# Optimization experiments

Measured on AMD Instinct MI355X. Metric: run time of the kernel, lower is better.

## Reference

```python
import jax, jax.numpy as jnp
import numpy as np

CLIP_MEAN = np.array([0.48145466, 0.4578275, 0.40821073], dtype=np.float32)
CLIP_STD = np.array([0.26862954, 0.26130258, 0.27577711], dtype=np.float32)


def setup_inputs() -> dict:
    key = jax.random.key(0)
    k_img, k_x, k_y, k_w, k_h = jax.random.split(key, 5)
    C, H, W = 3, 2048, 2048
    N = 256
    MAXB, MINB = 320, 32  # bbox side range in pixels
    img = jax.random.uniform(k_img, (C, H, W), dtype=jnp.float32, minval=0.0, maxval=255.0)
    x0 = jax.random.randint(k_x, (N,), 0, W - MAXB)
    y0 = jax.random.randint(k_y, (N,), 0, H - MAXB)
    bw = jax.random.randint(k_w, (N,), MINB, MAXB)
    bh = jax.random.randint(k_h, (N,), MINB, MAXB)
    bboxes = jnp.stack([x0, y0, x0 + bw, y0 + bh], axis=1).astype(jnp.int32)  # [N,4] xyxy
    return {
        "img": img,
        "mean": jnp.asarray(CLIP_MEAN),
        "std": jnp.asarray(CLIP_STD),
        "bboxes": bboxes,
        "size": 224,
    }


def _crop_resize(img, bboxes, size):
    """Batched crop-to-bbox + short-edge resize + center-crop == sample the
    central square (side = min(bh, bw)) of each bbox onto a size x size grid
    with bilinear interpolation. img: [C,H,W] float, bboxes: [N,4] int xyxy.
    Returns [N,C,size,size]."""
    C, H, W = img.shape
    b = bboxes.astype(jnp.float32)
    x0, y0, x1, y1 = b[:, 0], b[:, 1], b[:, 2], b[:, 3]
    side = jnp.minimum(x1 - x0, y1 - y0)            # [N]
    cx, cy = (x0 + x1) * 0.5, (y0 + y1) * 0.5        # [N]
    # output pixel j -> source coord start + (j+0.5)*scale - 0.5 (torch resize convention)
    grid = (jnp.arange(size, dtype=jnp.float32) + 0.5) / size  # [S]
    sx = (cx - side * 0.5)[:, None] + grid[None, :] * side[:, None] - 0.5  # [N,S]
    sy = (cy - side * 0.5)[:, None] + grid[None, :] * side[:, None] - 0.5  # [N,S]
    sx = jnp.clip(sx, 0.0, W - 1.0)
    sy = jnp.clip(sy, 0.0, H - 1.0)
    ix0 = jnp.floor(sx).astype(jnp.int32)
    iy0 = jnp.floor(sy).astype(jnp.int32)
    ix1 = jnp.minimum(ix0 + 1, W - 1)
    iy1 = jnp.minimum(iy0 + 1, H - 1)
    wx = (sx - ix0.astype(jnp.float32))[None, :, None, :]  # broadcast over C and y
    wy = (sy - iy0.astype(jnp.float32))[None, :, :, None]  # broadcast over C and x
    # gathers -> [C,N,S,S]
    p00 = img[:, iy0[:, :, None], ix0[:, None, :]]
    p01 = img[:, iy0[:, :, None], ix1[:, None, :]]
    p10 = img[:, iy1[:, :, None], ix0[:, None, :]]
    p11 = img[:, iy1[:, :, None], ix1[:, None, :]]
    top = p00 + wx * (p01 - p00)
    bot = p10 + wx * (p11 - p10)
    patches = top + wy * (bot - top)                 # [C,N,S,S]
    return jnp.transpose(patches, (1, 0, 2, 3))      # [N,C,S,S]


def reference(img, mean, std, bboxes, size):
    patches = _crop_resize(img, bboxes, size)        # [N,3,S,S]
    patches = patches / 255.0                        # ToFloat scaling
    return (patches - mean[None, :, None, None]) / std[None, :, None, None]
```

## Files before the change

### kernel.cpp

```cpp
#include <hip/hip_runtime.h>


#define S      224
#define IMG_H  2048
#define IMG_W  2048
#define PLANE  (IMG_H * IMG_W)

typedef float vfloat4 __attribute__((ext_vector_type(4)));
typedef float f32x2 __attribute__((ext_vector_type(2), aligned(4)));

__global__ __launch_bounds__(256) void patch_kernel(
    const float* __restrict__ img,
    const float* __restrict__ mean,
    const float* __restrict__ stdd,
    const int*   __restrict__ bboxes,
    float*       __restrict__ out)
{
    const int n   = blockIdx.y;
    const int idx = blockIdx.x * 256 + threadIdx.x;
    const int oy  = idx / 56;
    const int ox  = (idx - oy * 56) * 4;

    const int4 bb = ((const int4*)bboxes)[n];
    const float x0 = (float)bb.x;
    const float y0 = (float)bb.y;
    const float x1 = (float)bb.z;
    const float y1 = (float)bb.w;

    const float side  = fminf(x1 - x0, y1 - y0);
    const float basex = (x0 + x1) * 0.5f - side * 0.5f - 0.5f;
    const float basey = (y0 + y1) * 0.5f - side * 0.5f - 0.5f;
    const float invS  = 1.0f / (float)S;

    float sy = fmaf((oy + 0.5f) * invS, side, basey);
    sy = fminf(fmaxf(sy, 0.0f), (float)(IMG_H - 1));
    const int   iy0 = (int)floorf(sy);
    const int   iy1 = min(iy0 + 1, IMG_H - 1);
    const float wy  = sy - (float)iy0;

    int   ix0[4];
    float wx[4];
#pragma unroll
    for (int j = 0; j < 4; ++j) {
        float sx = fmaf((ox + j + 0.5f) * invS, side, basex);
        sx = fminf(fmaxf(sx, 0.0f), (float)(IMG_W - 1));
        ix0[j] = (int)floorf(sx);
        wx[j]  = sx - (float)ix0[j];
    }

    const int r0 = iy0 * IMG_W;
    const int r1 = iy1 * IMG_W;

    float sc[3], bs[3];
#pragma unroll
    for (int c = 0; c < 3; ++c) {
        const float sd = stdd[c];
        sc[c] = 1.0f / (255.0f * sd);
        bs[c] = -mean[c] / sd;
    }

#pragma unroll
    for (int c = 0; c < 3; ++c) {
        const float* __restrict__ pr0 = img + (size_t)c * PLANE + r0;
        const float* __restrict__ pr1 = img + (size_t)c * PLANE + r1;

        f32x2 q0[4], q1[4];
#pragma unroll
        for (int j = 0; j < 4; ++j) {
            q0[j] = *(const f32x2*)(pr0 + ix0[j]);
            q1[j] = *(const f32x2*)(pr1 + ix0[j]);
        }

        vfloat4 v;
#pragma unroll
        for (int j = 0; j < 4; ++j) {
            const float top = fmaf(wx[j], q0[j].y - q0[j].x, q0[j].x);
            const float bot = fmaf(wx[j], q1[j].y - q1[j].x, q1[j].x);
            const float val = fmaf(wy, bot - top, top);
            v[j] = fmaf(val, sc[c], bs[c]);
        }

        __builtin_nontemporal_store(
            v, (vfloat4*)(out + (size_t)(n * 3 + c) * (S * S) + (size_t)idx * 4));
    }
}

extern "C" void kernel_launch(void* const* d_in, const int* in_sizes, int n_in,
                              void* d_out, int out_size, void* d_ws, size_t ws_size,
                              hipStream_t stream)
{
    const float* img    = (const float*)d_in[0];
    const float* mean   = (const float*)d_in[1];
    const float* stdd   = (const float*)d_in[2];
    const int*   bboxes = (const int*)d_in[3];
    float* out = (float*)d_out;

    const int N = in_sizes[3] / 4;
    dim3 grid(S * S / (256 * 4), N);
    patch_kernel<<<grid, 256, 0, stream>>>(img, mean, stdd, bboxes, out);
}
```

Baseline: 234.4 us.

## Repack image into fp16 interleaved HWC layout before bilinear gather

Adds a pre-pass that converts the CHW fp32 image into a padded 4-channel fp16 HWC buffer in the workspace, so each bilinear tap reads all three channels for two adjacent pixels in one 16-byte load instead of three separate channel-plane loads. This cuts the number of scattered gather requests and the bytes fetched per sample. In exchange it adds a full-image repack pass (48MB read, 32MB written) on every call, and fp16 storage of 0-255 values introduces rounding error. The original CHW kernel is kept as a fallback when the workspace is too small.

After: 211.4 us. 1.11x faster.

```diff
diff --git a/kernel.cpp b/kernel.cpp
--- a/kernel.cpp
+++ b/kernel.cpp
@@ -7,10 +7,30 @@
 #define PLANE  (IMG_H * IMG_W)
 
 typedef float vfloat4 __attribute__((ext_vector_type(4)));
-typedef float f32x2 __attribute__((ext_vector_type(2), aligned(4)));
+typedef float f32x2  __attribute__((ext_vector_type(2), aligned(4)));
+typedef _Float16 f16x8 __attribute__((ext_vector_type(8), aligned(8)));
+
+__global__ __launch_bounds__(256) void repack_kernel(
+    const float* __restrict__ img, _Float16* __restrict__ hwc)
+{
+    const int i = (blockIdx.x * 256 + threadIdx.x) * 4;
+    const vfloat4 r = *(const vfloat4*)(img + 0 * PLANE + i);
+    const vfloat4 g = *(const vfloat4*)(img + 1 * PLANE + i);
+    const vfloat4 b = *(const vfloat4*)(img + 2 * PLANE + i);
+
+    f16x8 lo, hi;
+    lo[0] = (_Float16)r.x; lo[1] = (_Float16)g.x; lo[2] = (_Float16)b.x; lo[3] = (_Float16)0.f;
+    lo[4] = (_Float16)r.y; lo[5] = (_Float16)g.y; lo[6] = (_Float16)b.y; lo[7] = (_Float16)0.f;
+    hi[0] = (_Float16)r.z; hi[1] = (_Float16)g.z; hi[2] = (_Float16)b.z; hi[3] = (_Float16)0.f;
+    hi[4] = (_Float16)r.w; hi[5] = (_Float16)g.w; hi[6] = (_Float16)b.w; hi[7] = (_Float16)0.f;
+
+    _Float16* dst = hwc + (size_t)i * 4;
+    *(f16x8*)(dst)     = lo;
+    *(f16x8*)(dst + 8) = hi;
+}
 
 __global__ __launch_bounds__(256) void patch_kernel(
-    const float* __restrict__ img,
+    const _Float16* __restrict__ hwc,
     const float* __restrict__ mean,
     const float* __restrict__ stdd,
     const int*   __restrict__ bboxes,
@@ -48,8 +68,15 @@
         wx[j]  = sx - (float)ix0[j];
     }
 
-    const int r0 = iy0 * IMG_W;
-    const int r1 = iy1 * IMG_W;
+    const size_t r0 = (size_t)iy0 * IMG_W;
+    const size_t r1 = (size_t)iy1 * IMG_W;
+
+    f16x8 t0[4], t1[4];
+#pragma unroll
+    for (int j = 0; j < 4; ++j) {
+        t0[j] = *(const f16x8*)(hwc + (r0 + (size_t)ix0[j]) * 4);
+        t1[j] = *(const f16x8*)(hwc + (r1 + (size_t)ix0[j]) * 4);
+    }
 
     float sc[3], bs[3];
 #pragma unroll
@@ -61,27 +88,79 @@
 
 #pragma unroll
     for (int c = 0; c < 3; ++c) {
+        vfloat4 v;
+#pragma unroll
+        for (int j = 0; j < 4; ++j) {
+            const float p00 = (float)t0[j][c];
+            const float p01 = (float)t0[j][4 + c];
+            const float p10 = (float)t1[j][c];
+            const float p11 = (float)t1[j][4 + c];
+            const float top = fmaf(wx[j], p01 - p00, p00);
+            const float bot = fmaf(wx[j], p11 - p10, p10);
+            const float val = fmaf(wy, bot - top, top);
+            v[j] = fmaf(val, sc[c], bs[c]);
+        }
+        __builtin_nontemporal_store(
+            v, (vfloat4*)(out + (size_t)(n * 3 + c) * (S * S) + (size_t)idx * 4));
+    }
+}
+
+__global__ __launch_bounds__(256) void patch_kernel_chw(
+    const float* __restrict__ img,
+    const float* __restrict__ mean,
+    const float* __restrict__ stdd,
+    const int*   __restrict__ bboxes,
+    float*       __restrict__ out)
+{
+    const int n   = blockIdx.y;
+    const int idx = blockIdx.x * 256 + threadIdx.x;
+    const int oy  = idx / 56;
+    const int ox  = (idx - oy * 56) * 4;
+
+    const int4 bb = ((const int4*)bboxes)[n];
+    const float x0 = (float)bb.x, y0 = (float)bb.y, x1 = (float)bb.z, y1 = (float)bb.w;
+    const float side  = fminf(x1 - x0, y1 - y0);
+    const float basex = (x0 + x1) * 0.5f - side * 0.5f - 0.5f;
+    const float basey = (y0 + y1) * 0.5f - side * 0.5f - 0.5f;
+    const float invS  = 1.0f / (float)S;
+
+    float sy = fmaf((oy + 0.5f) * invS, side, basey);
+    sy = fminf(fmaxf(sy, 0.0f), (float)(IMG_H - 1));
+    const int   iy0 = (int)floorf(sy);
+    const int   iy1 = min(iy0 + 1, IMG_H - 1);
+    const float wy  = sy - (float)iy0;
+
+    int ix0[4]; float wx[4];
+#pragma unroll
+    for (int j = 0; j < 4; ++j) {
+        float sx = fmaf((ox + j + 0.5f) * invS, side, basex);
+        sx = fminf(fmaxf(sx, 0.0f), (float)(IMG_W - 1));
+        ix0[j] = (int)floorf(sx);
+        wx[j]  = sx - (float)ix0[j];
+    }
+
+    const int r0 = iy0 * IMG_W;
+    const int r1 = iy1 * IMG_W;
+
+    float sc[3], bs[3];
+#pragma unroll
+    for (int c = 0; c < 3; ++c) { const float sd = stdd[c]; sc[c] = 1.0f/(255.0f*sd); bs[c] = -mean[c]/sd; }
+
+#pragma unroll
+    for (int c = 0; c < 3; ++c) {
         const float* __restrict__ pr0 = img + (size_t)c * PLANE + r0;
         const float* __restrict__ pr1 = img + (size_t)c * PLANE + r1;
-
         f32x2 q0[4], q1[4];
 #pragma unroll
-        for (int j = 0; j < 4; ++j) {
-            q0[j] = *(const f32x2*)(pr0 + ix0[j]);
-            q1[j] = *(const f32x2*)(pr1 + ix0[j]);
-        }
-
+        for (int j = 0; j < 4; ++j) { q0[j] = *(const f32x2*)(pr0 + ix0[j]); q1[j] = *(const f32x2*)(pr1 + ix0[j]); }
         vfloat4 v;
 #pragma unroll
         for (int j = 0; j < 4; ++j) {
             const float top = fmaf(wx[j], q0[j].y - q0[j].x, q0[j].x);
             const float bot = fmaf(wx[j], q1[j].y - q1[j].x, q1[j].x);
-            const float val = fmaf(wy, bot - top, top);
-            v[j] = fmaf(val, sc[c], bs[c]);
+            v[j] = fmaf(fmaf(wy, bot - top, top), sc[c], bs[c]);
         }
-
-        __builtin_nontemporal_store(
-            v, (vfloat4*)(out + (size_t)(n * 3 + c) * (S * S) + (size_t)idx * 4));
+        __builtin_nontemporal_store(v, (vfloat4*)(out + (size_t)(n * 3 + c) * (S * S) + (size_t)idx * 4));
     }
 }
 
@@ -96,6 +175,15 @@
     float* out = (float*)d_out;
 
     const int N = in_sizes[3] / 4;
-    dim3 grid(S * S / (256 * 4), N);
-    patch_kernel<<<grid, 256, 0, stream>>>(img, mean, stdd, bboxes, out);
+    const size_t hwc_bytes = (size_t)PLANE * 4 * sizeof(_Float16);
+
+    if (d_ws != nullptr && ws_size >= hwc_bytes) {
+        _Float16* hwc = (_Float16*)d_ws;
+        repack_kernel<<<dim3(PLANE / (256 * 4)), 256, 0, stream>>>(img, hwc);
+        dim3 grid(S * S / (256 * 4), N);
+        patch_kernel<<<grid, 256, 0, stream>>>(hwc, mean, stdd, bboxes, out);
+    } else {
+        dim3 grid(S * S / (256 * 4), N);
+        patch_kernel_chw<<<grid, 256, 0, stream>>>(img, mean, stdd, bboxes, out);
+    }
 }
```

## Stage bbox source rows in LDS as interleaved fp16 RGB before bilinear sampling

Applied to the files above, without the earlier changes.

Each block now covers eight output rows of one patch. It first cooperatively loads the needed source rows for all three channels with vector loads and packs them into shared memory as fp16 RGBx quads. After a barrier, each thread gathers its four bilinear taps per output pixel from LDS instead of issuing scattered global loads. This is meant to remove redundant, uncoalesced global gathers, at the cost of fp16 rounding of the 0-255 pixel values and a block-wide sync. Source widths wider than the LDS row are clamped, which risks wrong results for very wide bboxes.

Result: faster. 208.4 us (-11.1%).

```diff
diff --git a/kernel.cpp b/kernel.cpp
--- a/kernel.cpp
+++ b/kernel.cpp
@@ -1,25 +1,31 @@
 #include <hip/hip_runtime.h>
 
 
-#define S      224
-#define IMG_H  2048
-#define IMG_W  2048
-#define PLANE  (IMG_H * IMG_W)
+#define S       224
+#define IMG_H   2048
+#define IMG_W   2048
+#define PLANE   (IMG_H * IMG_W)
+#define TILE_Y  8
+#define NTHREADS 448
+#define NROWS_MAX 14
+#define LDS_W   328
 
-typedef float vfloat4 __attribute__((ext_vector_type(4)));
-typedef float f32x2 __attribute__((ext_vector_type(2), aligned(4)));
+typedef float   vfloat4 __attribute__((ext_vector_type(4)));
+typedef _Float16 f16x4  __attribute__((ext_vector_type(4), aligned(8)));
+typedef _Float16 f16x8  __attribute__((ext_vector_type(8), aligned(16)));
 
-__global__ __launch_bounds__(256) void patch_kernel(
+__global__ __launch_bounds__(NTHREADS) void patch_kernel(
     const float* __restrict__ img,
     const float* __restrict__ mean,
     const float* __restrict__ stdd,
     const int*   __restrict__ bboxes,
     float*       __restrict__ out)
 {
+    __shared__ _Float16 lds[NROWS_MAX * LDS_W * 4];
+
     const int n   = blockIdx.y;
-    const int idx = blockIdx.x * 256 + threadIdx.x;
-    const int oy  = idx / 56;
-    const int ox  = (idx - oy * 56) * 4;
+    const int oy0 = blockIdx.x * TILE_Y;
+    const int tid = threadIdx.x;
 
     const int4 bb = ((const int4*)bboxes)[n];
     const float x0 = (float)bb.x;
@@ -32,24 +38,68 @@
     const float basey = (y0 + y1) * 0.5f - side * 0.5f - 0.5f;
     const float invS  = 1.0f / (float)S;
 
+    float sy_lo = fmaf((oy0 + 0.5f) * invS, side, basey);
+    float sy_hi = fmaf((oy0 + TILE_Y - 1 + 0.5f) * invS, side, basey);
+    sy_lo = fminf(fmaxf(sy_lo, 0.0f), (float)(IMG_H - 1));
+    sy_hi = fminf(fmaxf(sy_hi, 0.0f), (float)(IMG_H - 1));
+    const int ys0   = (int)floorf(sy_lo);
+    const int ys1   = min((int)floorf(sy_hi) + 1, IMG_H - 1);
+    const int nrows = min(ys1 - ys0 + 1, NROWS_MAX);
+
+    float sx_lo = fmaf(0.5f * invS, side, basex);
+    float sx_hi = fmaf((S - 1 + 0.5f) * invS, side, basex);
+    sx_lo = fminf(fmaxf(sx_lo, 0.0f), (float)(IMG_W - 1));
+    sx_hi = fminf(fmaxf(sx_hi, 0.0f), (float)(IMG_W - 1));
+    const int xs0a = ((int)floorf(sx_lo)) & ~3;
+    const int xs1  = min((int)floorf(sx_hi) + 1, IMG_W - 1);
+    const int nx4  = min((xs1 - xs0a + 4) >> 2, LDS_W / 4);
+
+    const int units = nrows * nx4;
+    for (int u = tid; u < units; u += NTHREADS) {
+        const int ri = u / nx4;
+        const int xi = u - ri * nx4;
+        const int xg = xs0a + xi * 4;
+        const int xgc = min(xg, IMG_W - 4);
+        const float* base = img + (size_t)(ys0 + ri) * IMG_W + xgc;
+        const vfloat4 r = *(const vfloat4*)(base);
+        const vfloat4 g = *(const vfloat4*)(base + PLANE);
+        const vfloat4 b = *(const vfloat4*)(base + 2 * PLANE);
+
+        f16x8 lo, hi;
+        lo[0] = (_Float16)r.x; lo[1] = (_Float16)g.x; lo[2] = (_Float16)b.x; lo[3] = (_Float16)0.f;
+        lo[4] = (_Float16)r.y; lo[5] = (_Float16)g.y; lo[6] = (_Float16)b.y; lo[7] = (_Float16)0.f;
+        hi[0] = (_Float16)r.z; hi[1] = (_Float16)g.z; hi[2] = (_Float16)b.z; hi[3] = (_Float16)0.f;
+        hi[4] = (_Float16)r.w; hi[5] = (_Float16)g.w; hi[6] = (_Float16)b.w; hi[7] = (_Float16)0.f;
+
+        f16x8* dst = (f16x8*)&lds[(size_t)(ri * LDS_W + xi * 4) * 4];
+        dst[0] = lo;
+        dst[1] = hi;
+    }
+    __syncthreads();
+
+    const int r  = tid / 56;
+    const int xq = tid - r * 56;
+    const int oy = oy0 + r;
+    const int ox = xq * 4;
+
     float sy = fmaf((oy + 0.5f) * invS, side, basey);
     sy = fminf(fmaxf(sy, 0.0f), (float)(IMG_H - 1));
     const int   iy0 = (int)floorf(sy);
     const int   iy1 = min(iy0 + 1, IMG_H - 1);
     const float wy  = sy - (float)iy0;
+    const int ry0 = min(max(iy0 - ys0, 0), nrows - 1);
+    const int ry1 = min(max(iy1 - ys0, 0), nrows - 1);
 
-    int   ix0[4];
+    int   lx[4];
     float wx[4];
 #pragma unroll
     for (int j = 0; j < 4; ++j) {
         float sx = fmaf((ox + j + 0.5f) * invS, side, basex);
         sx = fminf(fmaxf(sx, 0.0f), (float)(IMG_W - 1));
-        ix0[j] = (int)floorf(sx);
-        wx[j]  = sx - (float)ix0[j];
+        const int ix0 = (int)floorf(sx);
+        wx[j] = sx - (float)ix0;
+        lx[j] = min(max(ix0 - xs0a, 0), LDS_W - 2);
     }
-
-    const int r0 = iy0 * IMG_W;
-    const int r1 = iy1 * IMG_W;
 
     float sc[3], bs[3];
 #pragma unroll
@@ -59,29 +109,30 @@
         bs[c] = -mean[c] / sd;
     }
 
+    vfloat4 vc[3];
+#pragma unroll
+    for (int j = 0; j < 4; ++j) {
+        const f16x4 a0 = *(const f16x4*)&lds[(size_t)(ry0 * LDS_W + lx[j]) * 4];
+        const f16x4 a1 = *(const f16x4*)&lds[(size_t)(ry0 * LDS_W + lx[j] + 1) * 4];
+        const f16x4 b0 = *(const f16x4*)&lds[(size_t)(ry1 * LDS_W + lx[j]) * 4];
+        const f16x4 b1 = *(const f16x4*)&lds[(size_t)(ry1 * LDS_W + lx[j] + 1) * 4];
+#pragma unroll
+        for (int c = 0; c < 3; ++c) {
+            const float p00 = (float)a0[c];
+            const float p01 = (float)a1[c];
+            const float p10 = (float)b0[c];
+            const float p11 = (float)b1[c];
+            const float top = fmaf(wx[j], p01 - p00, p00);
+            const float bot = fmaf(wx[j], p11 - p10, p10);
+            const float val = fmaf(wy, bot - top, top);
+            vc[c][j] = fmaf(val, sc[c], bs[c]);
+        }
+    }
+
 #pragma unroll
     for (int c = 0; c < 3; ++c) {
-        const float* __restrict__ pr0 = img + (size_t)c * PLANE + r0;
-        const float* __restrict__ pr1 = img + (size_t)c * PLANE + r1;
-
-        f32x2 q0[4], q1[4];
-#pragma unroll
-        for (int j = 0; j < 4; ++j) {
-            q0[j] = *(const f32x2*)(pr0 + ix0[j]);
-            q1[j] = *(const f32x2*)(pr1 + ix0[j]);
-        }
-
-        vfloat4 v;
-#pragma unroll
-        for (int j = 0; j < 4; ++j) {
-            const float top = fmaf(wx[j], q0[j].y - q0[j].x, q0[j].x);
-            const float bot = fmaf(wx[j], q1[j].y - q1[j].x, q1[j].x);
-            const float val = fmaf(wy, bot - top, top);
-            v[j] = fmaf(val, sc[c], bs[c]);
-        }
-
         __builtin_nontemporal_store(
-            v, (vfloat4*)(out + (size_t)(n * 3 + c) * (S * S) + (size_t)idx * 4));
+            vc[c], (vfloat4*)(out + ((size_t)(n * 3 + c) * S + oy) * S + ox));
     }
 }
 
@@ -96,6 +147,6 @@
     float* out = (float*)d_out;
 
     const int N = in_sizes[3] / 4;
-    dim3 grid(S * S / (256 * 4), N);
-    patch_kernel<<<grid, 256, 0, stream>>>(img, mean, stdd, bboxes, out);
+    dim3 grid(S / TILE_Y, N);
+    patch_kernel<<<grid, NTHREADS, 0, stream>>>(img, mean, stdd, bboxes, out);
 }
```
